# Performance work log

Measured on AMD Instinct MI355X. Metric: run time of the kernel, lower is better.

## Reference

```python
import jax, jax.numpy as jnp
import numpy as np
from jax import lax

VOCAB, EMB, HID = 300, 128, 512  # num_embeddings, char_emb_dim, lstm_hidden_dim


def _run_lstm(x, mask, Wih, Whh, b, reverse):
    """Mask-aware unidirectional LSTM matching packed-sequence semantics.
    x: [B,T,D] float, mask: [B,T] float {0,1}. Returns [B,T,H] with padded
    positions zeroed (as pad_packed_sequence produces)."""
    B = x.shape[0]
    H = Whh.shape[1]
    xg = jnp.einsum('btd,gd->btg', x, Wih) + b  # precompute input projections [B,T,4H]

    def step(carry, inp):
        h, c = carry
        g, m = inp  # g:[B,4H], m:[B,1]
        gates = g + h @ Whh.T
        i, f, gg, o = jnp.split(gates, 4, axis=-1)  # torch gate order i,f,g,o
        i = jax.nn.sigmoid(i)
        f = jax.nn.sigmoid(f)
        gg = jnp.tanh(gg)
        o = jax.nn.sigmoid(o)
        c_new = f * c + i * gg
        h_new = o * jnp.tanh(c_new)
        # only advance state on valid tokens (packed-sequence behavior)
        h = jnp.where(m > 0, h_new, h)
        c = jnp.where(m > 0, c_new, c)
        return (h, c), h * m

    m_t = jnp.swapaxes(mask, 0, 1)[..., None]  # [T,B,1]
    xs = (jnp.swapaxes(xg, 0, 1), m_t)
    z = jnp.zeros((B, H), dtype=x.dtype)
    _, ys = lax.scan(step, (z, z), xs, reverse=reverse)
    return jnp.swapaxes(ys, 0, 1)  # [B,T,H]


def setup_inputs() -> dict:
    key = jax.random.key(0)
    ks = jax.random.split(key, 10)
    B, T, W1 = 64, 512, 65
    s = 1.0 / np.sqrt(HID)
    inp = {
        'flair_ids': jax.random.randint(ks[0], (B, T), 0, VOCAB),
        'flair_attention_mask': jnp.ones((B, T), dtype=jnp.int64 if jax.config.jax_enable_x64 else jnp.int32),
        'flair_boundary': jnp.sort(jax.random.randint(ks[1], (B, W1), 0, T), axis=1),
        'emb': jax.random.normal(ks[2], (VOCAB, EMB), dtype=jnp.float32),
        'Wih_f': jax.random.uniform(ks[3], (4 * HID, EMB), minval=-s, maxval=s, dtype=jnp.float32),
        'Whh_f': jax.random.uniform(ks[4], (4 * HID, HID), minval=-s, maxval=s, dtype=jnp.float32),
        'b_f': jax.random.uniform(ks[5], (4 * HID,), minval=-s, maxval=s, dtype=jnp.float32),
        'Wih_b': jax.random.uniform(ks[6], (4 * HID, EMB), minval=-s, maxval=s, dtype=jnp.float32),
        'Whh_b': jax.random.uniform(ks[7], (4 * HID, HID), minval=-s, maxval=s, dtype=jnp.float32),
        'b_b': jax.random.uniform(ks[8], (4 * HID,), minval=-s, maxval=s, dtype=jnp.float32),
    }
    return inp


def reference(flair_ids, flair_attention_mask, flair_boundary,
              emb, Wih_f, Whh_f, b_f, Wih_b, Whh_b, b_b):
    mask = flair_attention_mask.astype(emb.dtype)  # [B,T]
    x = emb[flair_ids]  # [B,T,EMB]
    h_fwd = _run_lstm(x, mask, Wih_f, Whh_f, b_f, reverse=False)
    h_bwd = _run_lstm(x, mask, Wih_b, Whh_b, b_b, reverse=True)
    out = jnp.concatenate([h_fwd, h_bwd], axis=-1)  # [B,T,2H]

    # vectorized boundary gather + concat (replaces the Python double loop)
    i_idx = flair_boundary[:, :-1]  # [B,W]
    j_idx = flair_boundary[:, 1:]
    valid = (i_idx != -1) & (j_idx != -1)
    out_i = jnp.take_along_axis(out, jnp.clip(i_idx, 0)[:, :, None], axis=1)  # [B,W,2H]
    out_j = jnp.take_along_axis(out, jnp.clip(j_idx, 0)[:, :, None], axis=1)
    word_emb = jnp.concatenate([out_i, out_j], axis=-1)  # [B,W,4H]
    return jnp.where(valid[:, :, None], word_emb, 0.0)
```

## Files before the change

### kernel.cpp

```cpp
#include <hip/hip_runtime.h>

#define BB 64
#define TT 512
#define EE 128
#define HH 512
#define NGRP 4
#define BG 16
#define JW 16
#define NSLOT 132
#define LDH 520
#define LDE 136

typedef _Float16 f16;
typedef f16 f16x8 __attribute__((ext_vector_type(8)));
typedef float floatx4 __attribute__((ext_vector_type(4)));
typedef unsigned u32x4 __attribute__((ext_vector_type(4)));
typedef unsigned long long u64;

__device__ __forceinline__ float sigmf(float x) { return 1.f / (1.f + __expf(-x)); }
__device__ __forceinline__ float tanhfast(float x) { return 2.f / (1.f + __expf(-2.f * x)) - 1.f; }

__global__ __launch_bounds__(64) void build_map(const int* __restrict__ bnd,
                                                int* __restrict__ slotmap)
{
  __shared__ unsigned char need[TT];
  const int b = blockIdx.x;
  for (int i = threadIdx.x; i < TT; i += 64) need[i] = 0;
  __syncthreads();
  {
    const int w = threadIdx.x;
    const int iv = bnd[b * 65 + w];
    const int jv = bnd[b * 65 + w + 1];
    if (iv != -1 && jv != -1) {
      int ic = iv < 0 ? 0 : (iv > TT - 1 ? TT - 1 : iv);
      int jc = jv < 0 ? 0 : (jv > TT - 1 ? TT - 1 : jv);
      need[ic] = 1;
      need[jc] = 1;
    }
  }
  __syncthreads();
  if (threadIdx.x == 0) {
    int c = 0;
    for (int t = 0; t < TT; ++t) slotmap[b * TT + t] = need[t] ? (c++) : -1;
  }
}

__global__ __launch_bounds__(256, 1) void lstm_scan(
    const int* __restrict__ ids, const int* __restrict__ maskI,
    const float* __restrict__ emb,
    const float* __restrict__ Wih_f, const float* __restrict__ Whh_f, const float* __restrict__ b_f,
    const float* __restrict__ Wih_b, const float* __restrict__ Whh_b, const float* __restrict__ b_b,
    const int* __restrict__ slotmap,
    f16* __restrict__ h_g,
    f16* __restrict__ hist,
    unsigned* __restrict__ flags)
{
  __shared__ f16 sH[BG * LDH];
  __shared__ f16 sX[BG * LDE];
  __shared__ f16 hOut[BG * JW];

  const int tid = threadIdx.x;
  const int bid = blockIdx.x;
  const int dom = bid & 7;
  const int slice = bid >> 3;
  const int dir = dom & 1;
  const int grp = dom >> 1;

  const float* Wih = dir ? Wih_b : Wih_f;
  const float* Whh = dir ? Whh_b : Whh_f;
  const float* bv  = dir ? b_b   : b_f;

  const int lane = tid & 63;
  const int wave = tid >> 6;
  const int rloc = lane & 15;
  const int kg   = lane >> 4;
  const int rglob = wave * 16 + rloc;
  const int jloc  = rglob >> 2;
  const int q     = rglob & 3;
  const int mbase = kg * 4;
  const int growL = q * HH + slice * JW + jloc;
  const int gb = grp * BG;
  const int blw = tid >> 2;

  f16x8 wh[16];
  {
    const float* wr = Whh + (size_t)growL * HH + kg * 8;
    #pragma unroll
    for (int kk = 0; kk < 16; ++kk) {
      float4 a0 = *(const float4*)(wr + kk * 32);
      float4 a1 = *(const float4*)(wr + kk * 32 + 4);
      f16x8 v;
      v[0]=(f16)a0.x; v[1]=(f16)a0.y; v[2]=(f16)a0.z; v[3]=(f16)a0.w;
      v[4]=(f16)a1.x; v[5]=(f16)a1.y; v[6]=(f16)a1.z; v[7]=(f16)a1.w;
      wh[kk] = v;
    }
  }
  f16x8 wx[4];
  {
    const float* wr = Wih + (size_t)growL * EE + kg * 8;
    #pragma unroll
    for (int kk = 0; kk < 4; ++kk) {
      float4 a0 = *(const float4*)(wr + kk * 32);
      float4 a1 = *(const float4*)(wr + kk * 32 + 4);
      f16x8 v;
      v[0]=(f16)a0.x; v[1]=(f16)a0.y; v[2]=(f16)a0.z; v[3]=(f16)a0.w;
      v[4]=(f16)a1.x; v[5]=(f16)a1.y; v[6]=(f16)a1.z; v[7]=(f16)a1.w;
      wx[kk] = v;
    }
  }
  const float bsc = bv[growL];

  float cc[4] = {0.f, 0.f, 0.f, 0.f};
  float hh[4] = {0.f, 0.f, 0.f, 0.f};
  int wd = 3000000;

  const int xrow = tid >> 4;
  const int xc0 = (tid & 15) * 8;

  float m4c[4]; float mBc = 0.f; int slotBc = -1; int idxN = 0;
  {
    const int t0 = dir ? (TT - 1) : 0;
    #pragma unroll
    for (int i = 0; i < 4; ++i)
      m4c[i] = (float)maskI[(gb + mbase + i) * TT + t0];
    if (tid < 64) {
      mBc = (float)maskI[(gb + blw) * TT + t0];
      slotBc = slotmap[(gb + blw) * TT + t0];
    }
    idxN = ids[(gb + xrow) * TT + (dir ? (TT - 2) : 1)];
    for (int e = tid; e < BG * 64; e += 256) {
      const int row = e >> 6, ch = e & 63;
      uint4 z = make_uint4(0u, 0u, 0u, 0u);
      *(uint4*)(sH + row * LDH + ch * 8) = z;
    }
    const int idx0 = ids[(gb + xrow) * TT + t0];
    float4 x0 = *(const float4*)(emb + (size_t)idx0 * EE + xc0);
    float4 x1 = *(const float4*)(emb + (size_t)idx0 * EE + xc0 + 4);
    f16x8 xv;
    xv[0]=(f16)x0.x; xv[1]=(f16)x0.y; xv[2]=(f16)x0.z; xv[3]=(f16)x0.w;
    xv[4]=(f16)x1.x; xv[5]=(f16)x1.y; xv[6]=(f16)x1.z; xv[7]=(f16)x1.w;
    *(f16x8*)(sX + xrow * LDE + xc0) = xv;
  }
  __syncthreads();

  for (int s = 0; s < TT; ++s) {
    const int ns = s + 1;

    u32x4 hv[4];
    if (s > 0) {
      const f16* hq = h_g + (((size_t)(s & 1) * 2 + dir) * NGRP + grp) * BG * HH;
      #pragma unroll
      for (int p = 0; p < 4; ++p)
        asm volatile("global_load_dwordx4 %0, %1, off sc1"
                     : "=v"(hv[p]) : "v"(hq + (size_t)(p * 256 + tid) * 8) : "memory");
    }

    float4 px0, px1; float m4n[4] = {0.f,0.f,0.f,0.f}; float mBn = 0.f; int slotBn = -1;
    const int idxC = idxN;
    if (ns < TT) {
      const int tn = dir ? (TT - 1 - ns) : ns;
      if (ns + 1 < TT) idxN = ids[(gb + xrow) * TT + (dir ? (TT - 2 - ns) : (ns + 1))];
      px0 = *(const float4*)(emb + (size_t)idxC * EE + xc0);
      px1 = *(const float4*)(emb + (size_t)idxC * EE + xc0 + 4);
      #pragma unroll
      for (int i = 0; i < 4; ++i)
        m4n[i] = (float)maskI[(gb + mbase + i) * TT + tn];
      if (tid < 64) {
        mBn = (float)maskI[(gb + blw) * TT + tn];
        slotBn = slotmap[(gb + blw) * TT + tn];
      }
    }

    floatx4 acc0 = {0.f, 0.f, 0.f, 0.f};
    floatx4 acc1 = {0.f, 0.f, 0.f, 0.f};
    {
      const f16* aX = sX + rloc * LDE + kg * 8;
      f16x8 a0 = *(const f16x8*)(aX + 0 * 32);
      f16x8 a1 = *(const f16x8*)(aX + 1 * 32);
      f16x8 a2 = *(const f16x8*)(aX + 2 * 32);
      f16x8 a3 = *(const f16x8*)(aX + 3 * 32);
      acc0 = __builtin_amdgcn_mfma_f32_16x16x32_f16(a0, wx[0], acc0, 0, 0, 0);
      acc1 = __builtin_amdgcn_mfma_f32_16x16x32_f16(a1, wx[1], acc1, 0, 0, 0);
      acc0 = __builtin_amdgcn_mfma_f32_16x16x32_f16(a2, wx[2], acc0, 0, 0, 0);
      acc1 = __builtin_amdgcn_mfma_f32_16x16x32_f16(a3, wx[3], acc1, 0, 0, 0);
    }

    if (s > 0) {
      asm volatile("s_waitcnt vmcnt(0)" ::: "memory");
      __builtin_amdgcn_sched_barrier(0);
      #pragma unroll
      for (int p = 0; p < 4; ++p) {
        const int e = p * 256 + tid;
        const int row = e >> 6, ch = e & 63;
        *(u32x4*)(sH + row * LDH + ch * 8) = hv[p];
      }
    }
    __syncthreads();

    if (ns < TT) {
      f16x8 xv;
      xv[0]=(f16)px0.x; xv[1]=(f16)px0.y; xv[2]=(f16)px0.z; xv[3]=(f16)px0.w;
      xv[4]=(f16)px1.x; xv[5]=(f16)px1.y; xv[6]=(f16)px1.z; xv[7]=(f16)px1.w;
      *(f16x8*)(sX + xrow * LDE + xc0) = xv;
    }

    {
      const f16* aH = sH + rloc * LDH + kg * 8;
      #pragma unroll
      for (int kk = 0; kk < 16; kk += 2) {
        f16x8 a0 = *(const f16x8*)(aH + kk * 32);
        f16x8 a1 = *(const f16x8*)(aH + (kk + 1) * 32);
        acc0 = __builtin_amdgcn_mfma_f32_16x16x32_f16(a0, wh[kk], acc0, 0, 0, 0);
        acc1 = __builtin_amdgcn_mfma_f32_16x16x32_f16(a1, wh[kk + 1], acc1, 0, 0, 0);
      }
    }
    floatx4 acc = acc0 + acc1;

    #pragma unroll
    for (int i = 0; i < 4; ++i) {
      const float g0 = acc[i] + bsc;
      const float s1 = __shfl_xor(g0, 1, 64);
      const float s2 = __shfl_xor(g0, 2, 64);
      const float s3 = __shfl_xor(s1, 2, 64);
      float vi, vf, vg, vo;
      if (q == 0)      { vi = g0; vf = s1; vg = s2; vo = s3; }
      else if (q == 1) { vi = s1; vf = g0; vg = s3; vo = s2; }
      else if (q == 2) { vi = s2; vf = s3; vg = g0; vo = s1; }
      else             { vi = s3; vf = s2; vg = s1; vo = g0; }
      const float ig = sigmf(vi);
      const float fg = sigmf(vf);
      const float gt = tanhfast(vg);
      const float og = sigmf(vo);
      const float cn = fg * cc[i] + ig * gt;
      const float hn = og * tanhfast(cn);
      const float m = m4c[i];
      cc[i] = m > 0.f ? cn : cc[i];
      float hk = m > 0.f ? hn : hh[i];
      const f16 h16 = (f16)hk;
      hh[i] = (float)h16;
    }
    {
      const float hq_ = (q == 0) ? hh[0] : (q == 1) ? hh[1] : (q == 2) ? hh[2] : hh[3];
      hOut[(mbase + q) * JW + jloc] = (f16)hq_;
    }
    __syncthreads();

    u64 hv8 = 0ULL;
    if (tid < 64) {
      const int c0 = (tid & 3) * 4;
      hv8 = *(const u64*)(hOut + blw * JW + c0);
      if (ns < TT) {
        u64* hdst = (u64*)(h_g + (((size_t)(ns & 1) * 2 + dir) * NGRP + grp) * BG * HH
                           + blw * HH + slice * JW + c0);
        asm volatile("global_store_dwordx2 %0, %1, off sc1" :: "v"(hdst), "v"(hv8) : "memory");
      }
    }
    if (ns < TT) {
      asm volatile("s_waitcnt vmcnt(0)" ::: "memory");
      if (tid == 0)
        __hip_atomic_store(flags + dom * 32 + slice, (unsigned)ns,
                           __ATOMIC_RELAXED, __HIP_MEMORY_SCOPE_AGENT);
    }
    if (tid < 64 && slotBc >= 0) {
      const u64 hvm = mBc > 0.f ? hv8 : 0ULL;
      *(u64*)(hist + ((size_t)(dir * BB + gb + blw) * NSLOT + slotBc) * HH
              + slice * JW + (tid & 3) * 4) = hvm;
    }

    if (ns < TT) {
      const unsigned tgt = (unsigned)ns;
      const unsigned* fl = flags + dom * 32 + (lane & 31);
      for (;;) {
        const unsigned v = __hip_atomic_load(fl, __ATOMIC_RELAXED, __HIP_MEMORY_SCOPE_AGENT);
        if (__all((lane >= 32) | (v >= tgt))) break;
        if (--wd < 0) break;
        __builtin_amdgcn_s_sleep(1);
      }
      __builtin_amdgcn_sched_barrier(0);
      asm volatile("" ::: "memory");
    }

    #pragma unroll
    for (int i = 0; i < 4; ++i) m4c[i] = m4n[i];
    mBc = mBn; slotBc = slotBn;
  }
}

__global__ __launch_bounds__(256) void gather_out(
    const int* __restrict__ bnd, const int* __restrict__ slotmap,
    const f16* __restrict__ hist, float* __restrict__ out)
{
  const int bw = blockIdx.x;
  const int b = bw >> 6;
  const int w = bw & 63;
  const int k = threadIdx.x * 8;
  const int iv = bnd[b * 65 + w];
  const int jv = bnd[b * 65 + w + 1];
  const bool valid = (iv != -1) && (jv != -1);
  float* dst = out + (size_t)bw * 2048 + k;
  if (valid) {
    const int seg = k >> 9;
    int ts = (seg < 2) ? iv : jv;
    ts = ts < 0 ? 0 : (ts > TT - 1 ? TT - 1 : ts);
    const int dirn = seg & 1;
    const int slot = slotmap[b * TT + ts];
    const f16* src = hist + ((size_t)(dirn * BB + b) * NSLOT + slot) * HH + (k & 511);
    f16x8 v = *(const f16x8*)src;
    float4 o0 = make_float4((float)v[0], (float)v[1], (float)v[2], (float)v[3]);
    float4 o1 = make_float4((float)v[4], (float)v[5], (float)v[6], (float)v[7]);
    *(float4*)dst = o0;
    *(float4*)(dst + 4) = o1;
  } else {
    float4 z = make_float4(0.f, 0.f, 0.f, 0.f);
    *(float4*)dst = z;
    *(float4*)(dst + 4) = z;
  }
}

extern "C" void kernel_launch(void* const* d_in, const int* in_sizes, int n_in,
                              void* d_out, int out_size, void* d_ws, size_t ws_size,
                              hipStream_t stream)
{
  (void)in_sizes; (void)n_in; (void)out_size; (void)ws_size;
  const int* ids     = (const int*)d_in[0];
  const int* maskI   = (const int*)d_in[1];
  const int* bnd     = (const int*)d_in[2];
  const float* emb   = (const float*)d_in[3];
  const float* Wih_f = (const float*)d_in[4];
  const float* Whh_f = (const float*)d_in[5];
  const float* b_f   = (const float*)d_in[6];
  const float* Wih_b = (const float*)d_in[7];
  const float* Whh_b = (const float*)d_in[8];
  const float* b_b   = (const float*)d_in[9];

  char* ws = (char*)d_ws;
  unsigned* flags = (unsigned*)ws;
  int* slotmap    = (int*)(ws + 4096);
  f16* h_g        = (f16*)(ws + 4096 + 131072);
  f16* hist       = (f16*)(ws + 4096 + 131072 + 262144);

  hipMemsetAsync(flags, 0, 4096, stream);
  build_map<<<dim3(BB), dim3(64), 0, stream>>>(bnd, slotmap);
  lstm_scan<<<dim3(256), dim3(256), 0, stream>>>(ids, maskI, emb,
      Wih_f, Whh_f, b_f, Wih_b, Whh_b, b_b, slotmap, h_g, hist, flags);
  gather_out<<<dim3(BB * 64), dim3(256), 0, stream>>>(bnd, slotmap, hist, (float*)d_out);
}
```

Measured before the change: 1.899 ms.

## Tag exchanged hidden-state words with step number to drop store-wait before flag

Each f16 hidden value is stored in a 32-bit word whose upper half holds the step number. Readers validate the tags and re-poll any stale lines, so producers no longer wait for their stores to complete before publishing the flag. Flag polling moves to a single wave followed by a block barrier instead of all waves spinning. This doubles exchange traffic per step and adds a memset of the larger buffer, but aims to shorten the critical inter-block synchronization latency of each recurrent step.

After: 1.904 ms. Within noise of the previous version (+0.3%).

```diff
diff --git a/kernel.cpp b/kernel.cpp
--- a/kernel.cpp
+++ b/kernel.cpp
@@ -51,7 +51,7 @@
     const float* __restrict__ Wih_f, const float* __restrict__ Whh_f, const float* __restrict__ b_f,
     const float* __restrict__ Wih_b, const float* __restrict__ Whh_b, const float* __restrict__ b_b,
     const int* __restrict__ slotmap,
-    f16* __restrict__ h_g,
+    unsigned* __restrict__ h_g,
     f16* __restrict__ hist,
     unsigned* __restrict__ flags)
 {
@@ -113,6 +113,7 @@
   float cc[4] = {0.f, 0.f, 0.f, 0.f};
   float hh[4] = {0.f, 0.f, 0.f, 0.f};
   int wd = 3000000;
+  int budget = 500000;
 
   const int xrow = tid >> 4;
   const int xc0 = (tid & 15) * 8;
@@ -146,13 +147,13 @@
   for (int s = 0; s < TT; ++s) {
     const int ns = s + 1;
 
-    u32x4 hv[4];
+    u32x4 hv[8];
+    unsigned* hq = h_g + (((size_t)(s & 1) * 2 + dir) * NGRP + grp) * BG * HH;
     if (s > 0) {
-      const f16* hq = h_g + (((size_t)(s & 1) * 2 + dir) * NGRP + grp) * BG * HH;
-      #pragma unroll
-      for (int p = 0; p < 4; ++p)
+      #pragma unroll
+      for (int p = 0; p < 8; ++p)
         asm volatile("global_load_dwordx4 %0, %1, off sc1"
-                     : "=v"(hv[p]) : "v"(hq + (size_t)(p * 256 + tid) * 8) : "memory");
+                     : "=v"(hv[p]) : "v"(hq + p * 1024 + tid * 4) : "memory");
     }
 
     float4 px0, px1; float m4n[4] = {0.f,0.f,0.f,0.f}; float mBn = 0.f; int slotBn = -1;
@@ -186,13 +187,40 @@
     }
 
     if (s > 0) {
+      const unsigned tagrep = (unsigned)s << 16;
       asm volatile("s_waitcnt vmcnt(0)" ::: "memory");
       __builtin_amdgcn_sched_barrier(0);
-      #pragma unroll
-      for (int p = 0; p < 4; ++p) {
-        const int e = p * 256 + tid;
-        const int row = e >> 6, ch = e & 63;
-        *(u32x4*)(sH + row * LDH + ch * 8) = hv[p];
+      unsigned bad = 0;
+      #pragma unroll
+      for (int p = 0; p < 8; ++p) {
+        const unsigned d = ((hv[p][0] ^ tagrep) | (hv[p][1] ^ tagrep) |
+                           (hv[p][2] ^ tagrep) | (hv[p][3] ^ tagrep)) & 0xffff0000u;
+        bad |= (d ? 1u : 0u) << p;
+      }
+      while (__builtin_expect(bad != 0, 0)) {
+        if (--budget < 0) break;
+        #pragma unroll
+        for (int p = 0; p < 8; ++p)
+          if (bad & (1u << p))
+            asm volatile("global_load_dwordx4 %0, %1, off sc1"
+                         : "=v"(hv[p]) : "v"(hq + p * 1024 + tid * 4) : "memory");
+        asm volatile("s_waitcnt vmcnt(0)" ::: "memory");
+        unsigned nb = 0;
+        #pragma unroll
+        for (int p = 0; p < 8; ++p) {
+          const unsigned d = ((hv[p][0] ^ tagrep) | (hv[p][1] ^ tagrep) |
+                             (hv[p][2] ^ tagrep) | (hv[p][3] ^ tagrep)) & 0xffff0000u;
+          nb |= (d ? 1u : 0u) << p;
+        }
+        bad = nb;
+      }
+      __builtin_amdgcn_sched_barrier(0);
+      #pragma unroll
+      for (int p = 0; p < 8; ++p) {
+        const unsigned lo = (hv[p][0] & 0xffffu) | (hv[p][1] << 16);
+        const unsigned hi = (hv[p][2] & 0xffffu) | (hv[p][3] << 16);
+        const int i0 = p * 1024 + tid * 4;
+        *(u64*)(sH + (i0 >> 9) * LDH + (i0 & 511)) = ((u64)hi << 32) | lo;
       }
     }
     __syncthreads();
@@ -250,17 +278,20 @@
       const int c0 = (tid & 3) * 4;
       hv8 = *(const u64*)(hOut + blw * JW + c0);
       if (ns < TT) {
-        u64* hdst = (u64*)(h_g + (((size_t)(ns & 1) * 2 + dir) * NGRP + grp) * BG * HH
-                           + blw * HH + slice * JW + c0);
-        asm volatile("global_store_dwordx2 %0, %1, off sc1" :: "v"(hdst), "v"(hv8) : "memory");
-      }
-    }
-    if (ns < TT) {
-      asm volatile("s_waitcnt vmcnt(0)" ::: "memory");
-      if (tid == 0)
-        __hip_atomic_store(flags + dom * 32 + slice, (unsigned)ns,
-                           __ATOMIC_RELAXED, __HIP_MEMORY_SCOPE_AGENT);
-    }
+        const unsigned tg2 = (unsigned)ns << 16;
+        u32x4 ev;
+        ev[0] = tg2 | (unsigned)(hv8 & 0xffff);
+        ev[1] = tg2 | (unsigned)((hv8 >> 16) & 0xffff);
+        ev[2] = tg2 | (unsigned)((hv8 >> 32) & 0xffff);
+        ev[3] = tg2 | (unsigned)((hv8 >> 48) & 0xffff);
+        unsigned* hdst = h_g + (((size_t)(ns & 1) * 2 + dir) * NGRP + grp) * BG * HH
+                         + blw * HH + slice * JW + c0;
+        asm volatile("global_store_dwordx4 %0, %1, off sc1" :: "v"(hdst), "v"(ev) : "memory");
+      }
+    }
+    if (ns < TT && tid == 0)
+      __hip_atomic_store(flags + dom * 32 + slice, (unsigned)ns,
+                         __ATOMIC_RELAXED, __HIP_MEMORY_SCOPE_AGENT);
     if (tid < 64 && slotBc >= 0) {
       const u64 hvm = mBc > 0.f ? hv8 : 0ULL;
       *(u64*)(hist + ((size_t)(dir * BB + gb + blw) * NSLOT + slotBc) * HH
@@ -268,14 +299,19 @@
     }
 
     if (ns < TT) {
-      const unsigned tgt = (unsigned)ns;
-      const unsigned* fl = flags + dom * 32 + (lane & 31);
-      for (;;) {
-        const unsigned v = __hip_atomic_load(fl, __ATOMIC_RELAXED, __HIP_MEMORY_SCOPE_AGENT);
-        if (__all((lane >= 32) | (v >= tgt))) break;
-        if (--wd < 0) break;
-        __builtin_amdgcn_s_sleep(1);
-      }
+      if (wave == 0) {
+        const unsigned tgt = (unsigned)ns;
+        const unsigned* fl = flags + dom * 32 + (lane & 31);
+        for (;;) {
+          unsigned v = tgt;
+          if (lane < 32)
+            v = __hip_atomic_load(fl, __ATOMIC_RELAXED, __HIP_MEMORY_SCOPE_AGENT);
+          if (__all(v >= tgt)) break;
+          if (--wd < 0) break;
+          __builtin_amdgcn_s_sleep(2);
+        }
+      }
+      __syncthreads();
       __builtin_amdgcn_sched_barrier(0);
       asm volatile("" ::: "memory");
     }
@@ -336,10 +372,11 @@
   char* ws = (char*)d_ws;
   unsigned* flags = (unsigned*)ws;
   int* slotmap    = (int*)(ws + 4096);
-  f16* h_g        = (f16*)(ws + 4096 + 131072);
-  f16* hist       = (f16*)(ws + 4096 + 131072 + 262144);
-
-  hipMemsetAsync(flags, 0, 4096, stream);
+  unsigned* h_g   = (unsigned*)(ws + 4096 + 131072);
+  f16* hist       = (f16*)(ws + 4096 + 131072 + 1048576);
+
+  hipMemsetAsync(ws, 0, 4096, stream);
+  hipMemsetAsync(h_g, 0, 1048576, stream);
   build_map<<<dim3(BB), dim3(64), 0, stream>>>(bnd, slotmap);
   lstm_scan<<<dim3(256), dim3(256), 0, stream>>>(ids, maskI, emb,
       Wih_f, Whh_f, b_f, Wih_b, Whh_b, b_b, slotmap, h_g, hist, flags);
```
